# Kernel optimization log

Hardware: AMD Instinct MI355X
Metric: run time of the kernel (lower is better)

## Reference

```python
import jax, jax.numpy as jnp
import numpy as np

B, S, D = 4, 2048, 1024
H = 16
HD = D // H  # 64

def setup_inputs() -> dict:
    key = jax.random.key(0)
    ks = jax.random.split(key, 7)
    s = 0.02
    return {
        "x": jax.random.normal(ks[0], (B, S, D), dtype=jnp.float32),
        "Wq": jax.random.normal(ks[1], (D, D), dtype=jnp.float32) * s,
        "bq": jax.random.normal(ks[2], (D,), dtype=jnp.float32) * s,
        "Wk": jax.random.normal(ks[3], (D, D), dtype=jnp.float32) * s,
        "bk": jax.random.normal(ks[4], (D,), dtype=jnp.float32) * s,
        "Wv": jax.random.normal(ks[5], (D, D), dtype=jnp.float32) * s,
        "bv": jax.random.normal(ks[6], (D,), dtype=jnp.float32) * s,
    }

def reference(x, Wq, bq, Wk, bk, Wv, bv):
    bs, seq, _ = x.shape
    q = (x @ Wq.T + bq).reshape(bs, seq, H, HD).transpose(0, 2, 1, 3)  # [b,h,s,d]
    k = (x @ Wk.T + bk).reshape(bs, seq, H, HD).transpose(0, 2, 1, 3)
    v = (x @ Wv.T + bv).reshape(bs, seq, H, HD).transpose(0, 2, 1, 3)
    scores = jnp.einsum('bhqd,bhkd->bhqk', q, k) / jnp.sqrt(jnp.float32(HD))
    probs = jax.nn.softmax(scores, axis=-1)  # dropout p=0 -> identity
    att = jnp.einsum('bhqk,bhkd->bhqd', probs, v)
    return att.transpose(0, 2, 1, 3).reshape(bs, seq, H * HD)
```

## Files before the change

### kernel.cpp

```cpp
#include <hip/hip_runtime.h>

typedef __bf16 bf16x8 __attribute__((ext_vector_type(8)));
typedef float f32x4 __attribute__((ext_vector_type(4)));

#define BATCH 4
#define SEQ   2048
#define DIM   1024
#define NH    16
#define HD    64

__device__ __forceinline__ unsigned short f2bf(float f) {
  union { float f; unsigned u; } v; v.f = f;
  unsigned u = v.u;
  u += 0x7FFF + ((u >> 16) & 1);
  return (unsigned short)(u >> 16);
}

__device__ __forceinline__ void g2lds16(const unsigned short* g, unsigned short* l) {
  __builtin_amdgcn_global_load_lds(
      (const __attribute__((address_space(1))) unsigned int*)g,
      (__attribute__((address_space(3))) unsigned int*)l, 16, 0, 0);
}

__global__ __launch_bounds__(256) void cast_bf16_kernel(
    const float* __restrict__ in, unsigned short* __restrict__ out, int n8) {
  int i = blockIdx.x * 256 + threadIdx.x;
  if (i >= n8) return;
  const float4* p = (const float4*)in + (size_t)i * 2;
  float4 a = p[0], b = p[1];
  unsigned short r[8];
  r[0] = f2bf(a.x); r[1] = f2bf(a.y); r[2] = f2bf(a.z); r[3] = f2bf(a.w);
  r[4] = f2bf(b.x); r[5] = f2bf(b.y); r[6] = f2bf(b.z); r[7] = f2bf(b.w);
  *(uint4*)&out[(size_t)i * 8] = *(uint4*)r;
}

__global__ __launch_bounds__(256) void cast_w_kernel(
    const float* __restrict__ w0, const float* __restrict__ w1,
    const float* __restrict__ w2, unsigned short* __restrict__ o0,
    unsigned short* __restrict__ o1, unsigned short* __restrict__ o2, int n8) {
  const float* in = (blockIdx.y == 0) ? w0 : (blockIdx.y == 1) ? w1 : w2;
  unsigned short* out = (blockIdx.y == 0) ? o0 : (blockIdx.y == 1) ? o1 : o2;
  int i = blockIdx.x * 256 + threadIdx.x;
  if (i >= n8) return;
  const float4* p = (const float4*)in + (size_t)i * 2;
  float4 a = p[0], b = p[1];
  unsigned short r[8];
  r[0] = f2bf(a.x); r[1] = f2bf(a.y); r[2] = f2bf(a.z); r[3] = f2bf(a.w);
  r[4] = f2bf(b.x); r[5] = f2bf(b.y); r[6] = f2bf(b.z); r[7] = f2bf(b.w);
  *(uint4*)&out[(size_t)i * 8] = *(uint4*)r;
}

__global__ __launch_bounds__(256) void gemm_qkv(
    const unsigned short* __restrict__ A,
    const unsigned short* __restrict__ Wqp, const unsigned short* __restrict__ Wkp,
    const unsigned short* __restrict__ Wvp,
    const float* __restrict__ bqp, const float* __restrict__ bkp,
    const float* __restrict__ bvp,
    unsigned short* __restrict__ oq, unsigned short* __restrict__ ok,
    unsigned short* __restrict__ ov) {
  __shared__ unsigned short As[128 * 32];
  __shared__ unsigned short Bs[128 * 32];
  const int z = blockIdx.z;
  const unsigned short* W = (z == 0) ? Wqp : (z == 1) ? Wkp : Wvp;
  const float* bias        = (z == 0) ? bqp : (z == 1) ? bkp : bvp;
  unsigned short* outp     = (z == 0) ? oq  : (z == 1) ? ok  : ov;
  const int mode = (z == 2) ? 1 : 0;

  const int tid  = threadIdx.x;
  const int wave = tid >> 6;
  const int lane = tid & 63;
  const int lm   = lane & 15;
  const int qd   = lane >> 4;
  const int m0 = blockIdx.x * 128;
  const int n0 = blockIdx.y * 128;
  const int wm = (wave >> 1) * 64;
  const int wn = (wave & 1) * 64;

  const f32x4 zero = {0.f, 0.f, 0.f, 0.f};
  f32x4 acc[4][4];
#pragma unroll
  for (int i = 0; i < 4; ++i)
#pragma unroll
    for (int j = 0; j < 4; ++j) acc[i][j] = zero;

  const int srow = tid >> 2;
  const int scol = (tid & 3) * 8;

  for (int kt = 0; kt < DIM; kt += 32) {
    __syncthreads();
    g2lds16(&A[(size_t)(m0 + srow) * DIM + kt + scol],       &As[(size_t)tid * 8]);
    g2lds16(&A[(size_t)(m0 + 64 + srow) * DIM + kt + scol],  &As[2048 + (size_t)tid * 8]);
    g2lds16(&W[(size_t)(n0 + srow) * DIM + kt + scol],       &Bs[(size_t)tid * 8]);
    g2lds16(&W[(size_t)(n0 + 64 + srow) * DIM + kt + scol],  &Bs[2048 + (size_t)tid * 8]);
    __syncthreads();

    bf16x8 af[4], bfr[4];
#pragma unroll
    for (int i = 0; i < 4; ++i) af[i]  = *(const bf16x8*)&As[(wm + i * 16 + lm) * 32 + qd * 8];
#pragma unroll
    for (int j = 0; j < 4; ++j) bfr[j] = *(const bf16x8*)&Bs[(wn + j * 16 + lm) * 32 + qd * 8];
#pragma unroll
    for (int i = 0; i < 4; ++i)
#pragma unroll
      for (int j = 0; j < 4; ++j)
        acc[i][j] = __builtin_amdgcn_mfma_f32_16x16x32_bf16(af[i], bfr[j], acc[i][j], 0, 0, 0);
  }

#pragma unroll
  for (int j = 0; j < 4; ++j) {
    int col = n0 + wn + j * 16 + lm;
    float bb = bias[col];
    int h = col >> 6, hd = col & 63;
#pragma unroll
    for (int i = 0; i < 4; ++i) {
#pragma unroll
      for (int r = 0; r < 4; ++r) {
        int row = m0 + wm + i * 16 + qd * 4 + r;
        int b = row >> 11, s = row & 2047;
        float v = acc[i][j][r] + bb;
        size_t idx;
        if (mode == 0) idx = ((size_t)(b * NH + h) * SEQ + s) * HD + hd;
        else           idx = ((size_t)(b * NH + h) * HD + hd) * SEQ + s;
        outp[idx] = f2bf(v);
      }
    }
  }
}

#define LDP 72
__global__ __launch_bounds__(256, 4) void flash_kernel(
    const unsigned short* __restrict__ Qw, const unsigned short* __restrict__ Kw,
    const unsigned short* __restrict__ Vw, float* __restrict__ out) {
  __shared__ unsigned short Ks2[2 * 64 * 32];
  __shared__ unsigned short Vs2[2 * 64 * 32];
  __shared__ unsigned short Ps[128 * LDP];
  __shared__ float Ls[128];

  const int tid  = threadIdx.x;
  const int w    = tid >> 6;
  const int lane = tid & 63;
  const int lm   = lane & 15;
  const int qd   = lane >> 4;
  const int bh   = blockIdx.y;
  const int q0   = blockIdx.x * 128;

  const unsigned short* Qbase = Qw + (size_t)bh * (SEQ * HD);
  const unsigned short* Kbase = Kw + (size_t)bh * (SEQ * HD);
  const unsigned short* Vbase = Vw + (size_t)bh * (HD * SEQ);

  bf16x8 qf[2][2];
#pragma unroll
  for (int g = 0; g < 2; ++g)
#pragma unroll
    for (int h = 0; h < 2; ++h)
      qf[g][h] = *(const bf16x8*)&Qbase[(size_t)(q0 + w * 32 + g * 16 + lm) * HD + h * 32 + qd * 8];

  const f32x4 zero = {0.f, 0.f, 0.f, 0.f};
  f32x4 o[2][4];
#pragma unroll
  for (int g = 0; g < 2; ++g)
#pragma unroll
    for (int jn = 0; jn < 4; ++jn) o[g][jn] = zero;
  float psg[2] = {0.f, 0.f};

  const int srow = tid >> 2;
  const int scol = (tid & 3) * 8;
  const float EC = 0.18033688f;

  for (int kt = 0; kt < SEQ / 64; ++kt) {
    __syncthreads();
    g2lds16(&Kbase[(size_t)(kt * 64 + srow) * HD + scol],      &Ks2[(size_t)tid * 8]);
    g2lds16(&Kbase[(size_t)(kt * 64 + srow) * HD + 32 + scol], &Ks2[2048 + (size_t)tid * 8]);
    g2lds16(&Vbase[(size_t)srow * SEQ + kt * 64 + scol],       &Vs2[(size_t)tid * 8]);
    g2lds16(&Vbase[(size_t)srow * SEQ + kt * 64 + 32 + scol],  &Vs2[2048 + (size_t)tid * 8]);
    __syncthreads();

#pragma unroll
    for (int jk = 0; jk < 4; ++jk) {
      bf16x8 kf0 = *(const bf16x8*)&Ks2[(jk * 16 + lm) * 32 + qd * 8];
      bf16x8 kf1 = *(const bf16x8*)&Ks2[2048 + (jk * 16 + lm) * 32 + qd * 8];
      f32x4 st[2];
#pragma unroll
      for (int g = 0; g < 2; ++g) {
        st[g] = __builtin_amdgcn_mfma_f32_16x16x32_bf16(kf0, qf[g][0], zero, 0, 0, 0);
        st[g] = __builtin_amdgcn_mfma_f32_16x16x32_bf16(kf1, qf[g][1], st[g], 0, 0, 0);
      }
#pragma unroll
      for (int g = 0; g < 2; ++g) {
        float p0 = __builtin_amdgcn_exp2f(st[g][0] * EC);
        float p1 = __builtin_amdgcn_exp2f(st[g][1] * EC);
        float p2 = __builtin_amdgcn_exp2f(st[g][2] * EC);
        float p3 = __builtin_amdgcn_exp2f(st[g][3] * EC);
        psg[g] += (p0 + p1) + (p2 + p3);
        uint2 pk;
        pk.x = __builtin_amdgcn_perm(__float_as_uint(p1), __float_as_uint(p0), 0x07060302);
        pk.y = __builtin_amdgcn_perm(__float_as_uint(p3), __float_as_uint(p2), 0x07060302);
        *(uint2*)&Ps[(w * 32 + g * 16 + lm) * LDP + jk * 16 + qd * 4] = pk;
      }
    }

    asm volatile("s_waitcnt lgkmcnt(0)" ::: "memory");

#pragma unroll
    for (int h2 = 0; h2 < 2; ++h2) {
      bf16x8 pf0 = *(const bf16x8*)&Ps[(w * 32 + lm) * LDP + h2 * 32 + qd * 8];
      bf16x8 pf1 = *(const bf16x8*)&Ps[(w * 32 + 16 + lm) * LDP + h2 * 32 + qd * 8];
#pragma unroll
      for (int jn = 0; jn < 4; ++jn) {
        bf16x8 vf = *(const bf16x8*)&Vs2[h2 * 2048 + (jn * 16 + lm) * 32 + qd * 8];
        o[0][jn] = __builtin_amdgcn_mfma_f32_16x16x32_bf16(pf0, vf, o[0][jn], 0, 0, 0);
        o[1][jn] = __builtin_amdgcn_mfma_f32_16x16x32_bf16(pf1, vf, o[1][jn], 0, 0, 0);
      }
    }
  }

  float l0 = psg[0], l1 = psg[1];
  l0 += __shfl_xor(l0, 16); l0 += __shfl_xor(l0, 32);
  l1 += __shfl_xor(l1, 16); l1 += __shfl_xor(l1, 32);
  if (qd == 0) {
    Ls[w * 32 + lm]      = l0;
    Ls[w * 32 + 16 + lm] = l1;
  }
  asm volatile("s_waitcnt lgkmcnt(0)" ::: "memory");

  const int b = bh >> 4, hh = bh & 15;
#pragma unroll
  for (int g = 0; g < 2; ++g)
#pragma unroll
    for (int r = 0; r < 4; ++r) {
      float inv = 1.0f / Ls[w * 32 + g * 16 + qd * 4 + r];
      int qrow = q0 + w * 32 + g * 16 + qd * 4 + r;
#pragma unroll
      for (int jn = 0; jn < 4; ++jn)
        out[(size_t)(b * SEQ + qrow) * DIM + hh * HD + jn * 16 + lm] = o[g][jn][r] * inv;
    }
}

extern "C" void kernel_launch(void* const* d_in, const int* in_sizes, int n_in,
                              void* d_out, int out_size, void* d_ws, size_t ws_size,
                              hipStream_t stream) {
  const float* x  = (const float*)d_in[0];
  const float* Wq = (const float*)d_in[1];
  const float* bq = (const float*)d_in[2];
  const float* Wk = (const float*)d_in[3];
  const float* bk = (const float*)d_in[4];
  const float* Wv = (const float*)d_in[5];
  const float* bv = (const float*)d_in[6];
  float* out = (float*)d_out;

  unsigned short* ws = (unsigned short*)d_ws;
  const size_t XE = (size_t)BATCH * SEQ * DIM;
  const size_t WE = (size_t)DIM * DIM;
  unsigned short* xb  = ws;
  unsigned short* wqb = xb + XE;
  unsigned short* wkb = wqb + WE;
  unsigned short* wvb = wkb + WE;
  unsigned short* qb  = wvb + WE;
  unsigned short* kb  = qb + XE;
  unsigned short* vb  = kb + XE;

  cast_bf16_kernel<<<(int)(XE / 8 / 256), 256, 0, stream>>>(x, xb, (int)(XE / 8));
  dim3 cw((int)(WE / 8 / 256), 3);
  cast_w_kernel<<<cw, 256, 0, stream>>>(Wq, Wk, Wv, wqb, wkb, wvb, (int)(WE / 8));

  dim3 gg(64, 8, 3);
  gemm_qkv<<<gg, 256, 0, stream>>>(xb, wqb, wkb, wvb, bq, bk, bv, qb, kb, vb);

  dim3 fg(SEQ / 128, BATCH * NH);
  flash_kernel<<<fg, 256, 0, stream>>>(qb, kb, vb, out);
}
```

Measured before the change: 263.1 us.

## Double-buffer GEMM and flash loads, fuse casts, fold softmax scale into Wq

New measurement: 289.8 us. 10.1% more time.

```diff
diff --git a/kernel.cpp b/kernel.cpp
--- a/kernel.cpp
+++ b/kernel.cpp
@@ -8,6 +8,7 @@
 #define DIM   1024
 #define NH    16
 #define HD    64
+#define ECF   0.18033688f
 
 __device__ __forceinline__ unsigned short f2bf(float f) {
   union { float f; unsigned u; } v; v.f = f;
@@ -22,32 +23,25 @@
       (__attribute__((address_space(3))) unsigned int*)l, 16, 0, 0);
 }
 
-__global__ __launch_bounds__(256) void cast_bf16_kernel(
-    const float* __restrict__ in, unsigned short* __restrict__ out, int n8) {
+__global__ __launch_bounds__(256) void cast_all_kernel(
+    const float* __restrict__ x,  const float* __restrict__ Wq,
+    const float* __restrict__ Wk, const float* __restrict__ Wv,
+    unsigned short* __restrict__ xb,  unsigned short* __restrict__ wqb,
+    unsigned short* __restrict__ wkb, unsigned short* __restrict__ wvb) {
+  const int XG = (BATCH * SEQ * DIM) / 8;
+  const int WG = (DIM * DIM) / 8;
   int i = blockIdx.x * 256 + threadIdx.x;
-  if (i >= n8) return;
-  const float4* p = (const float4*)in + (size_t)i * 2;
+  const float* in; unsigned short* out; float sc = 1.0f; int off;
+  if (i < XG)               { in = x;  out = xb;  off = i; }
+  else if (i < XG + WG)     { in = Wq; out = wqb; off = i - XG; sc = ECF; }
+  else if (i < XG + 2 * WG) { in = Wk; out = wkb; off = i - XG - WG; }
+  else                      { in = Wv; out = wvb; off = i - XG - 2 * WG; }
+  const float4* p = (const float4*)in + (size_t)off * 2;
   float4 a = p[0], b = p[1];
   unsigned short r[8];
-  r[0] = f2bf(a.x); r[1] = f2bf(a.y); r[2] = f2bf(a.z); r[3] = f2bf(a.w);
-  r[4] = f2bf(b.x); r[5] = f2bf(b.y); r[6] = f2bf(b.z); r[7] = f2bf(b.w);
-  *(uint4*)&out[(size_t)i * 8] = *(uint4*)r;
-}
-
-__global__ __launch_bounds__(256) void cast_w_kernel(
-    const float* __restrict__ w0, const float* __restrict__ w1,
-    const float* __restrict__ w2, unsigned short* __restrict__ o0,
-    unsigned short* __restrict__ o1, unsigned short* __restrict__ o2, int n8) {
-  const float* in = (blockIdx.y == 0) ? w0 : (blockIdx.y == 1) ? w1 : w2;
-  unsigned short* out = (blockIdx.y == 0) ? o0 : (blockIdx.y == 1) ? o1 : o2;
-  int i = blockIdx.x * 256 + threadIdx.x;
-  if (i >= n8) return;
-  const float4* p = (const float4*)in + (size_t)i * 2;
-  float4 a = p[0], b = p[1];
-  unsigned short r[8];
-  r[0] = f2bf(a.x); r[1] = f2bf(a.y); r[2] = f2bf(a.z); r[3] = f2bf(a.w);
-  r[4] = f2bf(b.x); r[5] = f2bf(b.y); r[6] = f2bf(b.z); r[7] = f2bf(b.w);
-  *(uint4*)&out[(size_t)i * 8] = *(uint4*)r;
+  r[0] = f2bf(a.x * sc); r[1] = f2bf(a.y * sc); r[2] = f2bf(a.z * sc); r[3] = f2bf(a.w * sc);
+  r[4] = f2bf(b.x * sc); r[5] = f2bf(b.y * sc); r[6] = f2bf(b.z * sc); r[7] = f2bf(b.w * sc);
+  *(uint4*)&out[(size_t)off * 8] = *(uint4*)r;
 }
 
 __global__ __launch_bounds__(256) void gemm_qkv(
@@ -58,12 +52,13 @@
     const float* __restrict__ bvp,
     unsigned short* __restrict__ oq, unsigned short* __restrict__ ok,
     unsigned short* __restrict__ ov) {
-  __shared__ unsigned short As[128 * 32];
-  __shared__ unsigned short Bs[128 * 32];
-  const int z = blockIdx.z;
+  __shared__ unsigned short As[2][128 * 32];
+  __shared__ unsigned short Bs[2][128 * 32];
+  const int z = blockIdx.y % 3;
   const unsigned short* W = (z == 0) ? Wqp : (z == 1) ? Wkp : Wvp;
   const float* bias        = (z == 0) ? bqp : (z == 1) ? bkp : bvp;
   unsigned short* outp     = (z == 0) ? oq  : (z == 1) ? ok  : ov;
+  const float bsc          = (z == 0) ? ECF : 1.0f;
   const int mode = (z == 2) ? 1 : 0;
 
   const int tid  = threadIdx.x;
@@ -72,7 +67,7 @@
   const int lm   = lane & 15;
   const int qd   = lane >> 4;
   const int m0 = blockIdx.x * 128;
-  const int n0 = blockIdx.y * 128;
+  const int n0 = (blockIdx.y / 3) * 128;
   const int wm = (wave >> 1) * 64;
   const int wn = (wave & 1) * 64;
 
@@ -86,19 +81,28 @@
   const int srow = tid >> 2;
   const int scol = (tid & 3) * 8;
 
-  for (int kt = 0; kt < DIM; kt += 32) {
+  g2lds16(&A[(size_t)(m0 + srow) * DIM + scol],      &As[0][(size_t)tid * 8]);
+  g2lds16(&A[(size_t)(m0 + 64 + srow) * DIM + scol], &As[0][2048 + (size_t)tid * 8]);
+  g2lds16(&W[(size_t)(n0 + srow) * DIM + scol],      &Bs[0][(size_t)tid * 8]);
+  g2lds16(&W[(size_t)(n0 + 64 + srow) * DIM + scol], &Bs[0][2048 + (size_t)tid * 8]);
+
+  for (int it = 0; it < DIM / 32; ++it) {
+    const int cur = it & 1;
     __syncthreads();
-    g2lds16(&A[(size_t)(m0 + srow) * DIM + kt + scol],       &As[(size_t)tid * 8]);
-    g2lds16(&A[(size_t)(m0 + 64 + srow) * DIM + kt + scol],  &As[2048 + (size_t)tid * 8]);
-    g2lds16(&W[(size_t)(n0 + srow) * DIM + kt + scol],       &Bs[(size_t)tid * 8]);
-    g2lds16(&W[(size_t)(n0 + 64 + srow) * DIM + kt + scol],  &Bs[2048 + (size_t)tid * 8]);
-    __syncthreads();
+    if (it + 1 < DIM / 32) {
+      const int kt = (it + 1) * 32;
+      const int nb = cur ^ 1;
+      g2lds16(&A[(size_t)(m0 + srow) * DIM + kt + scol],      &As[nb][(size_t)tid * 8]);
+      g2lds16(&A[(size_t)(m0 + 64 + srow) * DIM + kt + scol], &As[nb][2048 + (size_t)tid * 8]);
+      g2lds16(&W[(size_t)(n0 + srow) * DIM + kt + scol],      &Bs[nb][(size_t)tid * 8]);
+      g2lds16(&W[(size_t)(n0 + 64 + srow) * DIM + kt + scol], &Bs[nb][2048 + (size_t)tid * 8]);
+    }
 
     bf16x8 af[4], bfr[4];
 #pragma unroll
-    for (int i = 0; i < 4; ++i) af[i]  = *(const bf16x8*)&As[(wm + i * 16 + lm) * 32 + qd * 8];
-#pragma unroll
-    for (int j = 0; j < 4; ++j) bfr[j] = *(const bf16x8*)&Bs[(wn + j * 16 + lm) * 32 + qd * 8];
+    for (int i = 0; i < 4; ++i) af[i]  = *(const bf16x8*)&As[cur][(wm + i * 16 + lm) * 32 + qd * 8];
+#pragma unroll
+    for (int j = 0; j < 4; ++j) bfr[j] = *(const bf16x8*)&Bs[cur][(wn + j * 16 + lm) * 32 + qd * 8];
 #pragma unroll
     for (int i = 0; i < 4; ++i)
 #pragma unroll
@@ -109,7 +113,7 @@
 #pragma unroll
   for (int j = 0; j < 4; ++j) {
     int col = n0 + wn + j * 16 + lm;
-    float bb = bias[col];
+    float bb = bias[col] * bsc;
     int h = col >> 6, hd = col & 63;
 #pragma unroll
     for (int i = 0; i < 4; ++i) {
@@ -128,11 +132,11 @@
 }
 
 #define LDP 72
-__global__ __launch_bounds__(256, 4) void flash_kernel(
+__global__ __launch_bounds__(256, 3) void flash_kernel(
     const unsigned short* __restrict__ Qw, const unsigned short* __restrict__ Kw,
     const unsigned short* __restrict__ Vw, float* __restrict__ out) {
-  __shared__ unsigned short Ks2[2 * 64 * 32];
-  __shared__ unsigned short Vs2[2 * 64 * 32];
+  __shared__ unsigned short Ks2[2][2 * 64 * 32];
+  __shared__ unsigned short Vs2[2][2 * 64 * 32];
   __shared__ unsigned short Ps[128 * LDP];
   __shared__ float Ls[128];
 
@@ -165,20 +169,28 @@
 
   const int srow = tid >> 2;
   const int scol = (tid & 3) * 8;
-  const float EC = 0.18033688f;
+
+  g2lds16(&Kbase[(size_t)srow * HD + scol],      &Ks2[0][(size_t)tid * 8]);
+  g2lds16(&Kbase[(size_t)srow * HD + 32 + scol], &Ks2[0][2048 + (size_t)tid * 8]);
+  g2lds16(&Vbase[(size_t)srow * SEQ + scol],      &Vs2[0][(size_t)tid * 8]);
+  g2lds16(&Vbase[(size_t)srow * SEQ + 32 + scol], &Vs2[0][2048 + (size_t)tid * 8]);
 
   for (int kt = 0; kt < SEQ / 64; ++kt) {
+    const int cur = kt & 1;
     __syncthreads();
-    g2lds16(&Kbase[(size_t)(kt * 64 + srow) * HD + scol],      &Ks2[(size_t)tid * 8]);
-    g2lds16(&Kbase[(size_t)(kt * 64 + srow) * HD + 32 + scol], &Ks2[2048 + (size_t)tid * 8]);
-    g2lds16(&Vbase[(size_t)srow * SEQ + kt * 64 + scol],       &Vs2[(size_t)tid * 8]);
-    g2lds16(&Vbase[(size_t)srow * SEQ + kt * 64 + 32 + scol],  &Vs2[2048 + (size_t)tid * 8]);
-    __syncthreads();
+    if (kt + 1 < SEQ / 64) {
+      const int nb = cur ^ 1;
+      const int k1 = (kt + 1) * 64;
+      g2lds16(&Kbase[(size_t)(k1 + srow) * HD + scol],       &Ks2[nb][(size_t)tid * 8]);
+      g2lds16(&Kbase[(size_t)(k1 + srow) * HD + 32 + scol],  &Ks2[nb][2048 + (size_t)tid * 8]);
+      g2lds16(&Vbase[(size_t)srow * SEQ + k1 + scol],        &Vs2[nb][(size_t)tid * 8]);
+      g2lds16(&Vbase[(size_t)srow * SEQ + k1 + 32 + scol],   &Vs2[nb][2048 + (size_t)tid * 8]);
+    }
 
 #pragma unroll
     for (int jk = 0; jk < 4; ++jk) {
-      bf16x8 kf0 = *(const bf16x8*)&Ks2[(jk * 16 + lm) * 32 + qd * 8];
-      bf16x8 kf1 = *(const bf16x8*)&Ks2[2048 + (jk * 16 + lm) * 32 + qd * 8];
+      bf16x8 kf0 = *(const bf16x8*)&Ks2[cur][(jk * 16 + lm) * 32 + qd * 8];
+      bf16x8 kf1 = *(const bf16x8*)&Ks2[cur][2048 + (jk * 16 + lm) * 32 + qd * 8];
       f32x4 st[2];
 #pragma unroll
       for (int g = 0; g < 2; ++g) {
@@ -187,10 +199,10 @@
       }
 #pragma unroll
       for (int g = 0; g < 2; ++g) {
-        float p0 = __builtin_amdgcn_exp2f(st[g][0] * EC);
-        float p1 = __builtin_amdgcn_exp2f(st[g][1] * EC);
-        float p2 = __builtin_amdgcn_exp2f(st[g][2] * EC);
-        float p3 = __builtin_amdgcn_exp2f(st[g][3] * EC);
+        float p0 = __builtin_amdgcn_exp2f(st[g][0]);
+        float p1 = __builtin_amdgcn_exp2f(st[g][1]);
+        float p2 = __builtin_amdgcn_exp2f(st[g][2]);
+        float p3 = __builtin_amdgcn_exp2f(st[g][3]);
         psg[g] += (p0 + p1) + (p2 + p3);
         uint2 pk;
         pk.x = __builtin_amdgcn_perm(__float_as_uint(p1), __float_as_uint(p0), 0x07060302);
@@ -207,7 +219,7 @@
       bf16x8 pf1 = *(const bf16x8*)&Ps[(w * 32 + 16 + lm) * LDP + h2 * 32 + qd * 8];
 #pragma unroll
       for (int jn = 0; jn < 4; ++jn) {
-        bf16x8 vf = *(const bf16x8*)&Vs2[h2 * 2048 + (jn * 16 + lm) * 32 + qd * 8];
+        bf16x8 vf = *(const bf16x8*)&Vs2[cur][h2 * 2048 + (jn * 16 + lm) * 32 + qd * 8];
         o[0][jn] = __builtin_amdgcn_mfma_f32_16x16x32_bf16(pf0, vf, o[0][jn], 0, 0, 0);
         o[1][jn] = __builtin_amdgcn_mfma_f32_16x16x32_bf16(pf1, vf, o[1][jn], 0, 0, 0);
       }
@@ -259,11 +271,11 @@
   unsigned short* kb  = qb + XE;
   unsigned short* vb  = kb + XE;
 
-  cast_bf16_kernel<<<(int)(XE / 8 / 256), 256, 0, stream>>>(x, xb, (int)(XE / 8));
-  dim3 cw((int)(WE / 8 / 256), 3);
-  cast_w_kernel<<<cw, 256, 0, stream>>>(Wq, Wk, Wv, wqb, wkb, wvb, (int)(WE / 8));
-
-  dim3 gg(64, 8, 3);
+  const int total_groups = (int)(XE / 8 + 3 * (WE / 8));
+  cast_all_kernel<<<total_groups / 256, 256, 0, stream>>>(
+      x, Wq, Wk, Wv, xb, wqb, wkb, wvb);
+
+  dim3 gg(64, 24);
   gemm_qkv<<<gg, 256, 0, stream>>>(xb, wqb, wkb, wvb, bq, bk, bv, qb, kb, vb);
 
   dim3 fg(SEQ / 128, BATCH * NH);
```
